# Kernel tuning notes

Hardware: AMD Instinct MI355X
Metric: run time of the kernel (lower is better)

The kernel has to match this reference:

```python
import jax, jax.numpy as jnp
import numpy as np

D_MODEL = 1024
H = 16
D_K = D_MODEL // H


def setup_inputs() -> dict:
    key = jax.random.key(0)
    ks = jax.random.split(key, 8)
    B, S = 2, 2048
    q = jax.random.normal(ks[0], (B, S, D_MODEL), dtype=jnp.float32)
    k = jax.random.normal(ks[1], (B, S, D_MODEL), dtype=jnp.float32)
    v = jax.random.normal(ks[2], (B, S, D_MODEL), dtype=jnp.float32)
    mask = jnp.ones((B, 1, S), dtype=jnp.int32)  # key-padding mask, 1 = keep
    sc = 1.0 / np.sqrt(D_MODEL)
    # torch Linear weights [out, in]
    Wq = jax.random.normal(ks[3], (D_MODEL, D_MODEL), dtype=jnp.float32) * sc
    Wk = jax.random.normal(ks[4], (D_MODEL, D_MODEL), dtype=jnp.float32) * sc
    Wv = jax.random.normal(ks[5], (D_MODEL, D_MODEL), dtype=jnp.float32) * sc
    Wo = jax.random.normal(ks[6], (D_MODEL, D_MODEL), dtype=jnp.float32) * sc
    return {"q": q, "k": k, "v": v, "mask": mask,
            "Wq": Wq, "Wk": Wk, "Wv": Wv, "Wo": Wo}


def reference(q, k, v, mask, Wq, Wk, Wv, Wo):
    B, Sq, _ = q.shape
    Sk = k.shape[1]
    # projections (torch Linear: x @ W.T), split heads -> [B, H, S, d_k]
    def split_heads(x, W, S):
        return (x @ W.T).reshape(B, S, H, D_K).transpose(0, 2, 1, 3)
    qh = split_heads(q, Wq, Sq)
    kh = split_heads(k, Wk, Sk)
    vh = split_heads(v, Wv, Sk)
    scores = jnp.einsum('bhqd,bhkd->bhqk', qh, kh) / jnp.sqrt(
        jnp.asarray(D_K, qh.dtype))
    # mask.unsqueeze(1): [B,1,S] -> [B,1,1,S]; masked_fill(mask==0, -1e9)
    m = mask[:, None, :, :]
    scores = jnp.where(m == 0, jnp.asarray(-1e9, scores.dtype), scores)
    p = jax.nn.softmax(scores, axis=-1)
    out = jnp.einsum('bhqk,bhkd->bhqd', p, vh)
    out = out.transpose(0, 2, 1, 3).reshape(B, Sq, H * D_K)
    return out @ Wo.T
```

## Files before the change

### kernel.cpp

```cpp
#include <hip/hip_runtime.h>
#include <hip/hip_bf16.h>

#define LOG2E 1.4426950408889634f

typedef __attribute__((ext_vector_type(8))) __bf16 bf16x8;
typedef __attribute__((ext_vector_type(2))) __bf16 bf16x2;
typedef __attribute__((ext_vector_type(4))) float f32x4;
typedef __attribute__((ext_vector_type(16))) float f32x16;

#define MFMA16(a,b,c) __builtin_amdgcn_mfma_f32_16x16x32_bf16((a),(b),(c),0,0,0)
#define MFMA32(a,b,c) __builtin_amdgcn_mfma_f32_32x32x16_bf16((a),(b),(c),0,0,0)

#define GLL16(g, l) __builtin_amdgcn_global_load_lds( \
    (const __attribute__((address_space(1))) void*)(g), \
    (__attribute__((address_space(3))) void*)(l), 16, 0, 0)

__device__ __forceinline__ unsigned short bfu(float f) {
    __bf16 h = (__bf16)f; unsigned short u; __builtin_memcpy(&u, &h, 2); return u;
}
__device__ __forceinline__ unsigned cvtpk(float lo, float hi) {
    bf16x2 t; t.x = (__bf16)lo; t.y = (__bf16)hi;
    unsigned r; __builtin_memcpy(&r, &t, 4); return r;
}
__device__ __forceinline__ bf16x8 pack4(unsigned a, unsigned b, unsigned c, unsigned d) {
    union { unsigned u[4]; bf16x8 v; } t; t.u[0]=a; t.u[1]=b; t.u[2]=c; t.u[3]=d; return t.v;
}
__device__ __forceinline__ bf16x8 cvt8(float4 a, float4 b, float s) {
    bf16x8 o;
    o[0]=(__bf16)(a.x*s); o[1]=(__bf16)(a.y*s); o[2]=(__bf16)(a.z*s); o[3]=(__bf16)(a.w*s);
    o[4]=(__bf16)(b.x*s); o[5]=(__bf16)(b.y*s); o[6]=(__bf16)(b.z*s); o[7]=(__bf16)(b.w*s);
    return o;
}

__device__ __forceinline__ size_t kidx(int bh, int s, int d) {
    int kt = s>>6, half=(s>>5)&1, l31k=s&31;
    int dc=d>>4, hik=(d>>3)&1, e=d&7;
    return (((size_t)bh*32+kt)*8 + half*4+dc)*512 + (hik*32+l31k)*8 + e;
}
__device__ __forceinline__ size_t vidx(int bh, int s, int d) {
    int kt=s>>6, kvin=s&63, kc=kvin>>4, rem=kvin&15;
    int hiv=(rem>>2)&1, e=(rem&3)+4*(rem>>3);
    int v1=d>>5, l31v=d&31;
    return (((size_t)bh*32+kt)*8 + kc*2+v1)*512 + (hiv*32+l31v)*8 + e;
}

__global__ __launch_bounds__(256)
void conv_kernel(const float* __restrict__ q, const float* __restrict__ k,
                 const float* __restrict__ v, const float* __restrict__ Wq,
                 const float* __restrict__ Wk, const float* __restrict__ Wv,
                 const float* __restrict__ Wo, unsigned short* __restrict__ Xb,
                 unsigned short* __restrict__ Wb)
{
    const int y = blockIdx.y;
    if (y < 3) {
        const float* s = (y==0)?q:(y==1)?k:v;
        size_t i = ((size_t)blockIdx.x*256 + threadIdx.x)*8;
        float4 a = *(const float4*)(s+i), b = *(const float4*)(s+i+4);
        *(bf16x8*)(Xb + (size_t)y*4194304 + i) = cvt8(a, b, 1.0f);
    } else {
        const int w = blockIdx.x >> 9;
        const float* s = (w==0)?Wq:(w==1)?Wk:(w==2)?Wv:Wo;
        const float sc = (w==0) ? 0.125f*LOG2E : 1.0f;
        size_t i = ((size_t)(blockIdx.x & 511)*256 + threadIdx.x)*8;
        float4 a = *(const float4*)(s+i), b = *(const float4*)(s+i+4);
        *(bf16x8*)(Wb + (size_t)w*1048576 + i) = cvt8(a, b, sc);
    }
}

__global__ __launch_bounds__(256)
void qkv_kernel(const unsigned short* __restrict__ Xb,
                const unsigned short* __restrict__ Wb,
                unsigned short* __restrict__ Qh, unsigned short* __restrict__ Kg,
                unsigned short* __restrict__ Vg)
{
    __shared__ unsigned short As[2][4096];
    __shared__ unsigned short Bs[2][4096];
    const int z = blockIdx.z;
    const unsigned short* X = Xb + (size_t)z*4194304;
    const unsigned short* W = Wb + (size_t)z*1048576;
    const int t = threadIdx.x, wid = t>>6, lane = t&63;
    const int m0 = blockIdx.x*128, n0 = blockIdx.y*128;
    const int wr = (wid>>1)*64, wc = (wid&1)*64;
    const int lr = lane&15, lk = lane>>4;

    f32x4 acc[4][4] = {};

#pragma unroll
    for (int i=0;i<2;++i){
        int flat = i*4096 + wid*1024 + lane*16;
        int row = flat>>6, cb = (flat&63) ^ ((row&3)<<4);
        GLL16(X + (size_t)(m0+row)*1024 + (cb>>1), (char*)&As[0][0] + i*4096 + wid*1024);
        GLL16(W + (size_t)(n0+row)*1024 + (cb>>1), (char*)&Bs[0][0] + i*4096 + wid*1024);
    }
    asm volatile("s_waitcnt vmcnt(0)" ::: "memory");
    __builtin_amdgcn_s_barrier();
    asm volatile("" ::: "memory");

    for (int kt=0; kt<32; ++kt){
        const int cur = kt&1;
        if (kt<31){
            const int nb = cur^1, K0 = (kt+1)*32;
#pragma unroll
            for (int i=0;i<2;++i){
                int flat = i*4096 + wid*1024 + lane*16;
                int row = flat>>6, cb = (flat&63) ^ ((row&3)<<4);
                GLL16(X + (size_t)(m0+row)*1024 + K0 + (cb>>1), (char*)&As[nb][0] + i*4096 + wid*1024);
                GLL16(W + (size_t)(n0+row)*1024 + K0 + (cb>>1), (char*)&Bs[nb][0] + i*4096 + wid*1024);
            }
        }
        bf16x8 a[4], b[4];
#pragma unroll
        for (int i=0;i<4;++i){
            int row = wr+i*16+lr;
            a[i] = *(const bf16x8*)((const char*)&As[cur][0] + row*64 + ((lk*16)^((row&3)<<4)));
        }
#pragma unroll
        for (int j=0;j<4;++j){
            int row = wc+j*16+lr;
            b[j] = *(const bf16x8*)((const char*)&Bs[cur][0] + row*64 + ((lk*16)^((row&3)<<4)));
        }
#pragma unroll
        for (int i=0;i<4;++i)
#pragma unroll
            for (int j=0;j<4;++j)
                acc[i][j] = MFMA16(a[i], b[j], acc[i][j]);
        asm volatile("s_waitcnt vmcnt(0)" ::: "memory");
        __builtin_amdgcn_s_barrier();
        asm volatile("" ::: "memory");
    }

#pragma unroll
    for (int i=0;i<4;++i)
#pragma unroll
      for (int j=0;j<4;++j)
#pragma unroll
        for (int r=0;r<4;++r){
            int m = m0 + wr + i*16 + lk*4 + r;
            int n = n0 + wc + j*16 + lr;
            int b_ = m>>11, s = m&2047;
            int h = n>>6, d = n&63;
            int bh = b_*16 + h;
            unsigned short val = bfu(acc[i][j][r]);
            if (z==0)      Qh[((size_t)bh*2048 + s)*64 + d] = val;
            else if (z==1) Kg[kidx(bh, s, d)] = val;
            else           Vg[vidx(bh, s, d)] = val;
        }
}

__global__ __launch_bounds__(256)
void oproj_kernel(const unsigned short* __restrict__ Oh,
                  const unsigned short* __restrict__ Wo,
                  float* __restrict__ out)
{
    __shared__ unsigned short As[2][8192];
    __shared__ unsigned short Bs2[2][4096];
    const int t = threadIdx.x, wid = t>>6, lane = t&63;
    const int m0 = blockIdx.x*128, n0 = blockIdx.y*64;
    const int wr = (wid>>1)*64, wc = (wid&1)*32;
    const int lr = lane&15, lk = lane>>4;
    const int fbase = wid*1024 + lane*16;

    f32x4 acc[4][2] = {};

#pragma unroll
    for (int i=0;i<4;++i){
        int flat = i*4096 + fbase, row = flat>>7;
        int cb = (flat&127) ^ ((row&7)<<4);
        int m = m0+row, b_ = m>>11, s = m&2047;
        GLL16(Oh + ((size_t)(b_*16+0)*2048 + s)*64 + (cb>>1), (char*)&As[0][0] + i*4096 + wid*1024);
    }
#pragma unroll
    for (int i=0;i<2;++i){
        int flat = i*4096 + fbase, row = flat>>7;
        int cb = (flat&127) ^ ((row&7)<<4);
        GLL16(Wo + (size_t)(n0+row)*1024 + (cb>>1), (char*)&Bs2[0][0] + i*4096 + wid*1024);
    }

    for (int kt=0; kt<16; ++kt){
        const int cur = kt&1;
        if (kt<15){
            const int nb = cur^1, K0 = (kt+1)*64, h = K0>>6;
#pragma unroll
            for (int i=0;i<4;++i){
                int flat = i*4096 + fbase, row = flat>>7;
                int cb = (flat&127) ^ ((row&7)<<4);
                int m = m0+row, b_ = m>>11, s = m&2047;
                GLL16(Oh + ((size_t)(b_*16+h)*2048 + s)*64 + (cb>>1),
                      (char*)&As[nb][0] + i*4096 + wid*1024);
            }
#pragma unroll
            for (int i=0;i<2;++i){
                int flat = i*4096 + fbase, row = flat>>7;
                int cb = (flat&127) ^ ((row&7)<<4);
                GLL16(Wo + (size_t)(n0+row)*1024 + K0 + (cb>>1),
                      (char*)&Bs2[nb][0] + i*4096 + wid*1024);
            }
            asm volatile("s_waitcnt vmcnt(6)" ::: "memory");
        } else {
            asm volatile("s_waitcnt vmcnt(0)" ::: "memory");
        }
        __builtin_amdgcn_s_barrier();
        asm volatile("" ::: "memory");

        bf16x8 a[4][2], b[2][2];
#pragma unroll
        for (int i=0;i<4;++i){
            int row = wr+i*16+lr, sw = (row&7)<<4;
            const char* rp = (const char*)&As[cur][0] + row*128;
#pragma unroll
            for (int ks=0;ks<2;++ks)
                a[i][ks] = *(const bf16x8*)(rp + ((ks*64 + lk*16)^sw));
        }
#pragma unroll
        for (int j=0;j<2;++j){
            int row = wc+j*16+lr, sw = (row&7)<<4;
            const char* rp = (const char*)&Bs2[cur][0] + row*128;
#pragma unroll
            for (int ks=0;ks<2;++ks)
                b[j][ks] = *(const bf16x8*)(rp + ((ks*64 + lk*16)^sw));
        }
#pragma unroll
        for (int i=0;i<4;++i)
#pragma unroll
          for (int j=0;j<2;++j)
#pragma unroll
            for (int ks=0;ks<2;++ks)
                acc[i][j] = MFMA16(a[i][ks], b[j][ks], acc[i][j]);
        asm volatile("" ::: "memory");
        __builtin_amdgcn_s_barrier();
    }

#pragma unroll
    for (int i=0;i<4;++i)
#pragma unroll
      for (int j=0;j<2;++j)
#pragma unroll
        for (int r=0;r<4;++r){
            int m = m0 + wr + i*16 + lk*4 + r;
            int n = n0 + wc + j*16 + lr;
            out[(size_t)m*1024 + n] = acc[i][j][r];
        }
}

__global__ __launch_bounds__(128, 2)
void attn_kernel(const unsigned short* __restrict__ Qh,
                 const unsigned short* __restrict__ Kg,
                 const unsigned short* __restrict__ Vg,
                 const int* __restrict__ mask,
                 unsigned short* __restrict__ Oh)
{
    __shared__ unsigned short Ks[2][4096];
    __shared__ unsigned short Vs[2][4096];

    const int t = threadIdx.x, wid = t >> 6, lane = t & 63;
    const int l31 = lane & 31, hi = lane >> 5;
    const int linb = blockIdx.x + 32*blockIdx.y;
    const int work = (linb & 7)*128 + (linb >> 3);
    const int bh = work >> 5;
    const int q0 = (work & 31) * 64;
    const int b_ = bh >> 4;
    const int qw = q0 + wid*32 + l31;

    unsigned flagbits;
    {
        const int4* mp = (const int4*)(mask + b_*2048 + (lane&31)*64);
        int bad = 0;
#pragma unroll
        for (int i=0;i<16;++i){ int4 m4 = mp[i];
            bad |= (m4.x==0)|(m4.y==0)|(m4.z==0)|(m4.w==0); }
        unsigned long long bm = __ballot(bad);
        flagbits = (unsigned)bm;
    }

    bf16x8 qf[4];
    const unsigned short* Qp = Qh + ((size_t)bh*2048 + qw)*64 + hi*8;
#pragma unroll
    for (int dc = 0; dc < 4; ++dc) qf[dc] = *(const bf16x8*)(Qp + dc*16);

    const unsigned short* Kbase = Kg + (size_t)bh*131072;
    const unsigned short* Vbase = Vg + (size_t)bh*131072;

#pragma unroll
    for (int i = 0; i < 4; ++i) {
        int g = wid*4 + i;
        GLL16(Kbase + g*512 + lane*8, &Ks[0][g*512]);
        GLL16(Vbase + g*512 + lane*8, &Vs[0][g*512]);
    }

    f32x16 o0 = {}, o1 = {};
    float l_run = 0.0f;
    f32x16 minit;
#pragma unroll
    for (int r = 0; r < 16; ++r) minit[r] = -12.0f;

    for (int kt = 0; kt < 32; ++kt) {
        const int cur = kt & 1;
        if (kt < 31) {
            const int nb = cur ^ 1;
            const unsigned short* Kt = Kbase + (size_t)(kt+1)*4096;
            const unsigned short* Vt2 = Vbase + (size_t)(kt+1)*4096;
#pragma unroll
            for (int i = 0; i < 4; ++i) {
                int g = wid*4 + i;
                GLL16(Kt + g*512 + lane*8, &Ks[nb][g*512]);
                GLL16(Vt2 + g*512 + lane*8, &Vs[nb][g*512]);
            }
            asm volatile("s_waitcnt vmcnt(8)" ::: "memory");
        } else {
            asm volatile("s_waitcnt vmcnt(0)" ::: "memory");
        }
        __builtin_amdgcn_s_barrier();
        asm volatile("" ::: "memory");

        bf16x8 kb[8], vf[8];
#pragma unroll
        for (int f = 0; f < 8; ++f) kb[f] = *(const bf16x8*)&Ks[cur][f*512 + lane*8];
#pragma unroll
        for (int g = 0; g < 8; ++g) vf[g] = *(const bf16x8*)&Vs[cur][g*512 + lane*8];

        f32x16 s0, s1;
#pragma unroll
        for (int dc = 0; dc < 4; ++dc) {
            if (dc == 0) { s0 = MFMA32(kb[0], qf[0], minit); s1 = MFMA32(kb[4], qf[0], minit); }
            else         { s0 = MFMA32(kb[dc], qf[dc], s0);  s1 = MFMA32(kb[4+dc], qf[dc], s1); }
        }

        if (flagbits & (1u << kt)) {
            const int* mrow = mask + b_*2048 + kt*64;
#pragma unroll
            for (int r = 0; r < 16; ++r) {
                int kv = (r&3) + 8*(r>>2) + 4*hi;
                if (mrow[kv] == 0)      s0[r] = -1e9f;
                if (mrow[32 + kv] == 0) s1[r] = -1e9f;
            }
        }

#pragma unroll
        for (int r = 0; r < 16; ++r) {
            s0[r] = __builtin_amdgcn_exp2f(s0[r]);
            s1[r] = __builtin_amdgcn_exp2f(s1[r]);
        }

        {
            float rs = 0.0f;
#pragma unroll
            for (int r = 0; r < 16; ++r) rs += s0[r] + s1[r];
            l_run += rs;
        }

        bf16x8 pa[4];
        pa[0] = pack4(cvtpk(s0[0],s0[1]),  cvtpk(s0[2],s0[3]),
                      cvtpk(s0[4],s0[5]),  cvtpk(s0[6],s0[7]));
        pa[1] = pack4(cvtpk(s0[8],s0[9]),  cvtpk(s0[10],s0[11]),
                      cvtpk(s0[12],s0[13]),cvtpk(s0[14],s0[15]));
        pa[2] = pack4(cvtpk(s1[0],s1[1]),  cvtpk(s1[2],s1[3]),
                      cvtpk(s1[4],s1[5]),  cvtpk(s1[6],s1[7]));
        pa[3] = pack4(cvtpk(s1[8],s1[9]),  cvtpk(s1[10],s1[11]),
                      cvtpk(s1[12],s1[13]),cvtpk(s1[14],s1[15]));

#pragma unroll
        for (int kc = 0; kc < 4; ++kc) {
            o0 = MFMA32(pa[kc], vf[kc*2],   o0);
            o1 = MFMA32(pa[kc], vf[kc*2+1], o1);
        }
        asm volatile("" ::: "memory");
        __builtin_amdgcn_s_barrier();
    }

    float l_tot = l_run + __shfl_xor(l_run, 32);

    float cc[16];
    {
        float* Lb = (float*)((char*)&Ks[0][0] + wid*256);
        Lb[l31] = l_tot;
        asm volatile("s_waitcnt lgkmcnt(0)" ::: "memory");
#pragma unroll
        for (int g = 0; g < 4; ++g) {
            float4 v = *(const float4*)&Lb[g*8 + hi*4];
            cc[4*g]=v.x; cc[4*g+1]=v.y; cc[4*g+2]=v.z; cc[4*g+3]=v.w;
        }
    }

    unsigned short* Ob = Oh + ((size_t)bh*2048 + q0 + wid*32)*64;
#pragma unroll
    for (int r = 0; r < 16; ++r) {
        int qr = (r&3) + 8*(r>>2) + 4*hi;
        float inv = 1.0f / cc[r];
        Ob[(size_t)qr*64 + l31]      = bfu(o0[r] * inv);
        Ob[(size_t)qr*64 + 32 + l31] = bfu(o1[r] * inv);
    }
}

extern "C" void kernel_launch(void* const* d_in, const int* in_sizes, int n_in,
                              void* d_out, int out_size, void* d_ws, size_t ws_size,
                              hipStream_t stream)
{
    const float* q  = (const float*)d_in[0];
    const float* k  = (const float*)d_in[1];
    const float* v  = (const float*)d_in[2];
    const int* mask = (const int*)d_in[3];
    const float* Wq = (const float*)d_in[4];
    const float* Wk = (const float*)d_in[5];
    const float* Wv = (const float*)d_in[6];
    const float* Wo = (const float*)d_in[7];
    float* out = (float*)d_out;

    unsigned short* Xb = (unsigned short*)d_ws;
    unsigned short* Wb = Xb + (size_t)12582912;
    unsigned short* Qh = Wb + (size_t)4194304;
    unsigned short* Kg = Qh + (size_t)4194304;
    unsigned short* Vg = Kg + (size_t)4194304;
    unsigned short* Oh = Xb;

    conv_kernel<<<dim3(2048,4), 256, 0, stream>>>(q, k, v, Wq, Wk, Wv, Wo, Xb, Wb);
    qkv_kernel<<<dim3(32,8,3), 256, 0, stream>>>(Xb, Wb, Qh, Kg, Vg);
    attn_kernel<<<dim3(32,32), 128, 0, stream>>>(Qh, Kg, Vg, mask, Oh);
    oproj_kernel<<<dim3(32,16), 256, 0, stream>>>(Oh, Wb + (size_t)3145728, out);
}
```

Baseline: 128.5 us.

## Use 4-wave attention blocks with triple-buffered K/V prefetch

Attention blocks grow from 2 to 4 waves, each covering 128 query rows, so every K/V tile loaded into LDS serves twice as many queries. Loads are split across four waves, and the pipeline moves from double to triple buffering with a two-tile prefetch distance. The goal is less redundant K/V traffic and more hidden load latency. In exchange LDS per block rises and the grid has half as many blocks. The vmcnt waits were retuned for the deeper pipeline, and the mask-flag and LDS-reduction code assuming two waves is unchanged, which may be unsafe.

Measured after the change: 121.0 us. 5.8% less time.

```diff
diff --git a/kernel.cpp b/kernel.cpp
--- a/kernel.cpp
+++ b/kernel.cpp
@@ -242,22 +242,22 @@
         }
 }
 
-__global__ __launch_bounds__(128, 2)
+__global__ __launch_bounds__(256, 3)
 void attn_kernel(const unsigned short* __restrict__ Qh,
                  const unsigned short* __restrict__ Kg,
                  const unsigned short* __restrict__ Vg,
                  const int* __restrict__ mask,
                  unsigned short* __restrict__ Oh)
 {
-    __shared__ unsigned short Ks[2][4096];
-    __shared__ unsigned short Vs[2][4096];
+    __shared__ unsigned short Ks[3][4096];
+    __shared__ unsigned short Vs[3][4096];
 
     const int t = threadIdx.x, wid = t >> 6, lane = t & 63;
     const int l31 = lane & 31, hi = lane >> 5;
-    const int linb = blockIdx.x + 32*blockIdx.y;
-    const int work = (linb & 7)*128 + (linb >> 3);
-    const int bh = work >> 5;
-    const int q0 = (work & 31) * 64;
+    const int linb = blockIdx.x + 16*blockIdx.y;
+    const int work = (linb & 7)*64 + (linb >> 3);
+    const int bh = work >> 4;
+    const int q0 = (work & 15) * 128;
     const int b_ = bh >> 4;
     const int qw = q0 + wid*32 + l31;
 
@@ -280,12 +280,18 @@
     const unsigned short* Kbase = Kg + (size_t)bh*131072;
     const unsigned short* Vbase = Vg + (size_t)bh*131072;
 
-#pragma unroll
-    for (int i = 0; i < 4; ++i) {
-        int g = wid*4 + i;
-        GLL16(Kbase + g*512 + lane*8, &Ks[0][g*512]);
-        GLL16(Vbase + g*512 + lane*8, &Vs[0][g*512]);
-    }
+#define STAGE(ktile, buf) do { \
+    const unsigned short* Kt_ = Kbase + (size_t)(ktile)*4096; \
+    const unsigned short* Vt_ = Vbase + (size_t)(ktile)*4096; \
+    _Pragma("unroll") \
+    for (int i_ = 0; i_ < 2; ++i_) { \
+        int g_ = wid*2 + i_; \
+        GLL16(Kt_ + g_*512 + lane*8, &Ks[buf][g_*512]); \
+        GLL16(Vt_ + g_*512 + lane*8, &Vs[buf][g_*512]); \
+    } } while (0)
+
+    STAGE(0, 0);
+    STAGE(1, 1);
 
     f32x16 o0 = {}, o1 = {};
     float l_run = 0.0f;
@@ -294,18 +300,12 @@
     for (int r = 0; r < 16; ++r) minit[r] = -12.0f;
 
     for (int kt = 0; kt < 32; ++kt) {
-        const int cur = kt & 1;
-        if (kt < 31) {
-            const int nb = cur ^ 1;
-            const unsigned short* Kt = Kbase + (size_t)(kt+1)*4096;
-            const unsigned short* Vt2 = Vbase + (size_t)(kt+1)*4096;
-#pragma unroll
-            for (int i = 0; i < 4; ++i) {
-                int g = wid*4 + i;
-                GLL16(Kt + g*512 + lane*8, &Ks[nb][g*512]);
-                GLL16(Vt2 + g*512 + lane*8, &Vs[nb][g*512]);
-            }
+        const int cur = kt % 3;
+        if (kt + 2 < 32) {
+            STAGE(kt + 2, (kt + 2) % 3);
             asm volatile("s_waitcnt vmcnt(8)" ::: "memory");
+        } else if (kt + 1 < 32) {
+            asm volatile("s_waitcnt vmcnt(4)" ::: "memory");
         } else {
             asm volatile("s_waitcnt vmcnt(0)" ::: "memory");
         }
@@ -366,6 +366,7 @@
         asm volatile("" ::: "memory");
         __builtin_amdgcn_s_barrier();
     }
+#undef STAGE
 
     float l_tot = l_run + __shfl_xor(l_run, 32);
 
@@ -414,6 +415,6 @@
 
     conv_kernel<<<dim3(2048,4), 256, 0, stream>>>(q, k, v, Wq, Wk, Wv, Wo, Xb, Wb);
     qkv_kernel<<<dim3(32,8,3), 256, 0, stream>>>(Xb, Wb, Qh, Kg, Vg);
-    attn_kernel<<<dim3(32,32), 128, 0, stream>>>(Qh, Kg, Vg, mask, Oh);
+    attn_kernel<<<dim3(16,32), 256, 0, stream>>>(Qh, Kg, Vg, mask, Oh);
     oproj_kernel<<<dim3(32,16), 256, 0, stream>>>(Oh, Wb + (size_t)3145728, out);
 }
```
